# Performance work log

Hardware: AMD Instinct MI355X
Metric: run time of the kernel (lower is better)

The kernel has to match this reference:

```python
import jax, jax.numpy as jnp
import numpy as np

N = 100_000      # nodes
E = 1_600_000    # directed edges (before self-loops)
F_IN = 256       # input node features
H = 128          # hidden_dim
HEADS = 2
C_HEAD = H // HEADS  # 64, GATConv out_channels per head
G = 128          # graphs in batch
NCLS = 10
NEG_SLOPE = 0.2  # PyG GATConv default


def setup_inputs() -> dict:
    key = jax.random.key(0)
    ks = jax.random.split(key, 20)
    p = lambda k, shape: (jax.random.normal(k, shape, jnp.float32) * 0.05)
    x = jax.random.normal(ks[0], (N, F_IN), jnp.float32)
    edge_index = jax.random.randint(ks[1], (2, E), 0, N, dtype=jnp.int64)
    batch = jnp.sort(jax.random.randint(ks[2], (N,), 0, G, dtype=jnp.int64))
    return dict(
        x=x, edge_index=edge_index, batch=batch,
        pre_w=p(ks[3], (F_IN, H)), pre_b=p(ks[4], (H,)),
        w1=p(ks[5], (H, H)), asrc1=p(ks[6], (HEADS, C_HEAD)), adst1=p(ks[7], (HEADS, C_HEAD)), b1=p(ks[8], (H,)),
        w2=p(ks[9], (H, H)), asrc2=p(ks[10], (HEADS, C_HEAD)), adst2=p(ks[11], (HEADS, C_HEAD)), b2=p(ks[12], (H,)),
        post_w1=p(ks[13], (H, H)), post_b1=p(ks[14], (H,)),
        post_w2=p(ks[15], (H, NCLS)), post_b2=p(ks[16], (NCLS,)),
    )


def _gat_conv(h_in, w, a_src, a_dst, b, src, dst):
    # h: [N, heads, c]
    h = (h_in @ w).reshape(N, HEADS, C_HEAD)
    alpha_src = jnp.sum(h * a_src, axis=-1)  # [N, heads]
    alpha_dst = jnp.sum(h * a_dst, axis=-1)  # [N, heads]
    e = jax.nn.leaky_relu(alpha_src[src] + alpha_dst[dst], NEG_SLOPE)  # [E+N, heads]
    # numerically stable softmax over incoming edges of each destination node
    m = jax.ops.segment_max(e, dst, num_segments=N)
    ex = jnp.exp(e - m[dst])
    denom = jax.ops.segment_sum(ex, dst, num_segments=N)
    alpha = ex / denom[dst]                                           # [E+N, heads]
    out = jax.ops.segment_sum(h[src] * alpha[:, :, None], dst, num_segments=N)
    return out.reshape(N, H) + b  # concat heads + bias


def reference(x, edge_index, batch, pre_w, pre_b,
              w1, asrc1, adst1, b1, w2, asrc2, adst2, b2,
              post_w1, post_b1, post_w2, post_b2):
    # PyG GATConv default add_self_loops=True
    loop = jnp.arange(N, dtype=edge_index.dtype)
    src = jnp.concatenate([edge_index[0], loop])
    dst = jnp.concatenate([edge_index[1], loop])

    h = jax.nn.relu(x @ pre_w + pre_b)
    reprs = jax.ops.segment_sum(h, batch, num_segments=G)
    h = jax.nn.relu(_gat_conv(h, w1, asrc1, adst1, b1, src, dst))
    reprs = reprs + jax.ops.segment_sum(h, batch, num_segments=G)
    h = jax.nn.relu(_gat_conv(h, w2, asrc2, adst2, b2, src, dst))
    reprs = reprs + jax.ops.segment_sum(h, batch, num_segments=G)
    z = jax.nn.relu(reprs @ post_w1 + post_b1) @ post_w2 + post_b2
    return jax.nn.log_softmax(z, axis=-1)
```

## Files before the change

### kernel.cpp

```cpp
#include <hip/hip_runtime.h>
#include <hip/hip_bf16.h>
#include <math.h>

#define NNODES 100000
#define NEDGES 1600000
#define FIN 256
#define HDIM 128
#define NGRAPH 128
#define NCLS 10
#define NEG 0.2f

#define NBUCK 98
#define EPB 4096
#define EBLK ((NEDGES + EPB - 1) / EPB)

typedef short bf8 __attribute__((ext_vector_type(8)));
typedef float f4 __attribute__((ext_vector_type(4)));

__device__ __forceinline__ float lrelu(float x) { return x > 0.f ? x : NEG * x; }

__device__ __forceinline__ unsigned short f2bf(float f) {
  union { float f; unsigned int u; } v; v.f = f;
  unsigned int r = v.u + 0x7fffu + ((v.u >> 16) & 1u);
  return (unsigned short)(r >> 16);
}
__device__ __forceinline__ float bf_lo(unsigned int p) {
  union { unsigned int u; float f; } v; v.u = p << 16; return v.f;
}
__device__ __forceinline__ float bf_hi(unsigned int p) {
  union { unsigned int u; float f; } v; v.u = p & 0xffff0000u; return v.f;
}

__global__ __launch_bounds__(256) void convert_transpose(const float* __restrict__ w,
                                                         unsigned short* __restrict__ wt,
                                                         int K) {
  int i = blockIdx.x * 256 + threadIdx.x;
  if (i >= K * 128) return;
  int k = i >> 7, n = i & 127;
  wt[n * K + k] = f2bf(w[(size_t)k * 128 + n]);
}

__global__ __launch_bounds__(256) void gemm_mfma(const float* __restrict__ A,
                                                 const unsigned short* __restrict__ Bt,
                                                 const float* __restrict__ bias,
                                                 float* __restrict__ C,
                                                 unsigned int* __restrict__ Cp,
                                                 const float* __restrict__ a_src,
                                                 const float* __restrict__ a_dst,
                                                 float* __restrict__ o_as,
                                                 float* __restrict__ o_ad,
                                                 int M, int K, int dorelu) {
  __shared__ bf8 As[512];
  __shared__ bf8 Bs[512];
  int tid = threadIdx.x;
  int wv = tid >> 6, lane = tid & 63;
  int quad = lane >> 4, m16 = lane & 15;
  int row0 = blockIdx.x * 128;

  f4 acc[2][8];
#pragma unroll
  for (int a = 0; a < 2; ++a)
#pragma unroll
    for (int b = 0; b < 8; ++b) acc[a][b] = (f4){0.f, 0.f, 0.f, 0.f};

  for (int kb = 0; kb < K; kb += 32) {
    __syncthreads();
#pragma unroll
    for (int bb = 0; bb < 2; ++bb) {
      int b = tid + bb * 256;
      int l = b & 63, mt = b >> 6;
      int row = row0 + mt * 16 + (l & 15);
      if (row > M - 1) row = M - 1;
      const float* src = &A[(size_t)row * K + kb + (l >> 4) * 8];
      float4 x0 = *reinterpret_cast<const float4*>(src);
      float4 x1 = *reinterpret_cast<const float4*>(src + 4);
      bf8 v;
      v[0] = (short)f2bf(x0.x); v[1] = (short)f2bf(x0.y);
      v[2] = (short)f2bf(x0.z); v[3] = (short)f2bf(x0.w);
      v[4] = (short)f2bf(x1.x); v[5] = (short)f2bf(x1.y);
      v[6] = (short)f2bf(x1.z); v[7] = (short)f2bf(x1.w);
      As[b] = v;
    }
#pragma unroll
    for (int bb = 0; bb < 2; ++bb) {
      int b = tid + bb * 256;
      int l = b & 63, tn = b >> 6;
      int n = tn * 16 + (l & 15);
      Bs[b] = *reinterpret_cast<const bf8*>(&Bt[(size_t)n * K + kb + (l >> 4) * 8]);
    }
    __syncthreads();
    bf8 af0 = As[(wv * 2 + 0) * 64 + lane];
    bf8 af1 = As[(wv * 2 + 1) * 64 + lane];
#pragma unroll
    for (int tn = 0; tn < 8; ++tn) {
      bf8 bfm = Bs[tn * 64 + lane];
      acc[0][tn] = __builtin_amdgcn_mfma_f32_16x16x32_bf16(af0, bfm, acc[0][tn], 0, 0, 0);
      acc[1][tn] = __builtin_amdgcn_mfma_f32_16x16x32_bf16(af1, bfm, acc[1][tn], 0, 0, 0);
    }
  }

  if (Cp) {
    if (a_src) {
      float aS[8], aD[8];
#pragma unroll
      for (int tn = 0; tn < 4; ++tn) {
        aS[tn]     = a_src[tn * 16 + m16];
        aS[tn + 4] = a_src[64 + tn * 16 + m16];
        aD[tn]     = a_dst[tn * 16 + m16];
        aD[tn + 4] = a_dst[64 + tn * 16 + m16];
      }
#pragma unroll
      for (int mt = 0; mt < 2; ++mt)
#pragma unroll
        for (int r = 0; r < 4; ++r) {
          int row = row0 + wv * 32 + mt * 16 + quad * 4 + r;
          float ps0 = 0.f, ps1 = 0.f, pd0 = 0.f, pd1 = 0.f;
#pragma unroll
          for (int tn = 0; tn < 4; ++tn) {
            float v0 = acc[mt][tn][r], v1 = acc[mt][tn + 4][r];
            ps0 = fmaf(v0, aS[tn], ps0);
            ps1 = fmaf(v1, aS[tn + 4], ps1);
            pd0 = fmaf(v0, aD[tn], pd0);
            pd1 = fmaf(v1, aD[tn + 4], pd1);
          }
#pragma unroll
          for (int o = 8; o; o >>= 1) {
            ps0 += __shfl_xor(ps0, o); ps1 += __shfl_xor(ps1, o);
            pd0 += __shfl_xor(pd0, o); pd1 += __shfl_xor(pd1, o);
          }
          if (m16 == 0 && row < M) {
            o_as[2 * row] = ps0; o_as[2 * row + 1] = ps1;
            o_ad[2 * row] = pd0; o_ad[2 * row + 1] = pd1;
          }
        }
    }
#pragma unroll
    for (int mt = 0; mt < 2; ++mt)
#pragma unroll
      for (int tn = 0; tn < 4; ++tn)
#pragma unroll
        for (int r = 0; r < 4; ++r) {
          int row = row0 + wv * 32 + mt * 16 + quad * 4 + r;
          if (row < M) {
            unsigned int p = (unsigned int)f2bf(acc[mt][tn][r]) |
                             ((unsigned int)f2bf(acc[mt][tn + 4][r]) << 16);
            Cp[(size_t)row * 64 + tn * 16 + m16] = p;
          }
        }
  } else {
#pragma unroll
    for (int mt = 0; mt < 2; ++mt)
#pragma unroll
      for (int tn = 0; tn < 8; ++tn) {
        float bv = bias ? bias[tn * 16 + m16] : 0.f;
#pragma unroll
        for (int r = 0; r < 4; ++r) {
          int row = row0 + wv * 32 + mt * 16 + quad * 4 + r;
          if (row < M) {
            float v = acc[mt][tn][r] + bv;
            if (dorelu) v = fmaxf(v, 0.f);
            C[(size_t)row * 128 + tn * 16 + m16] = v;
          }
        }
      }
  }
}

__global__ void find_starts(const int* __restrict__ batch, int* __restrict__ gstart) {
  int g = threadIdx.x;
  if (g > NGRAPH) return;
  if (g == NGRAPH) { gstart[g] = NNODES; return; }
  int lo = 0, hi = NNODES;
  while (lo < hi) { int mid = (lo + hi) >> 1; if (batch[mid] < g) lo = mid + 1; else hi = mid; }
  gstart[g] = lo;
}

__global__ __launch_bounds__(256) void bin_count(const int* __restrict__ edst,
                                                 int* __restrict__ blockHist) {
  __shared__ int hist[NBUCK];
  int t = threadIdx.x, blk = blockIdx.x;
  if (t < NBUCK) hist[t] = 0;
  __syncthreads();
  int e0 = blk * EPB;
#pragma unroll
  for (int it = 0; it < EPB / 256; ++it) {
    int e = e0 + it * 256 + t;
    if (e < NEDGES) atomicAdd(&hist[((unsigned)edst[e]) >> 10], 1);
  }
  __syncthreads();
  if (t < NBUCK) blockHist[blk * NBUCK + t] = hist[t];
}

__global__ __launch_bounds__(512) void colscan(const int* __restrict__ blockHist,
                                               int* __restrict__ blockBaseCol,
                                               int* __restrict__ bucket_total) {
  __shared__ int s[512];
  int b = blockIdx.x, t = threadIdx.x;
  int v = (t < EBLK) ? blockHist[t * NBUCK + b] : 0;
  s[t] = v;
  __syncthreads();
  for (int off = 1; off < 512; off <<= 1) {
    int u = (t >= off) ? s[t - off] : 0;
    __syncthreads();
    s[t] += u;
    __syncthreads();
  }
  if (t < EBLK) blockBaseCol[b * EBLK + t] = s[t] - v;
  if (t == 511) bucket_total[b] = s[511];
}

__global__ __launch_bounds__(128) void bscan(const int* __restrict__ bucket_total,
                                             int* __restrict__ bucket_ptr) {
  __shared__ int s[128];
  int t = threadIdx.x;
  int v = (t < NBUCK) ? bucket_total[t] : 0;
  s[t] = v;
  __syncthreads();
  for (int off = 1; off < 128; off <<= 1) {
    int u = (t >= off) ? s[t - off] : 0;
    __syncthreads();
    s[t] += u;
    __syncthreads();
  }
  if (t < NBUCK) bucket_ptr[t] = s[t] - v;
  if (t == 127) bucket_ptr[NBUCK] = s[127];
}

__global__ __launch_bounds__(512) void bin_place(const int* __restrict__ esrc,
                                                 const int* __restrict__ edst,
                                                 const int* __restrict__ blockBaseCol,
                                                 const int* __restrict__ bucket_ptr,
                                                 uint2* __restrict__ stagingG) {
  __shared__ int hist[NBUCK + 1], lbase[NBUCK + 1], lcur[NBUCK + 1], cbase[NBUCK];
  __shared__ int tmp[128];
  __shared__ uint2 st[EPB];
  int t = threadIdx.x, blk = blockIdx.x;
  if (t < NBUCK + 1) hist[t] = 0;
  __syncthreads();
  int e0 = blk * EPB;
#pragma unroll
  for (int it = 0; it < EPB / 512; ++it) {
    int e = e0 + it * 512 + t;
    int b = NBUCK;
    if (e < NEDGES) b = ((unsigned)edst[e]) >> 10;
    atomicAdd(&hist[b], 1);
  }
  __syncthreads();
  if (t < 128) tmp[t] = (t < NBUCK + 1) ? hist[t] : 0;
  __syncthreads();
  for (int off = 1; off < 128; off <<= 1) {
    int u = 0;
    if (t < 128 && t >= off) u = tmp[t - off];
    __syncthreads();
    if (t < 128) tmp[t] += u;
    __syncthreads();
  }
  if (t < NBUCK + 1) { int ex = tmp[t] - hist[t]; lbase[t] = ex; lcur[t] = ex; }
  if (t < NBUCK) cbase[t] = bucket_ptr[t] + blockBaseCol[t * EBLK + blk];
  __syncthreads();
#pragma unroll
  for (int it = 0; it < EPB / 512; ++it) {
    int e = e0 + it * 512 + t;
    unsigned s = 0, d = 0xFFFFFFFFu;
    if (e < NEDGES) { s = (unsigned)esrc[e]; d = (unsigned)edst[e]; }
    int b = (d == 0xFFFFFFFFu) ? NBUCK : (int)(d >> 10);
    int slot = atomicAdd(&lcur[b], 1);
    st[slot] = make_uint2(s, d);
  }
  __syncthreads();
  for (int i = t; i < EPB; i += 512) {
    uint2 ed = st[i];
    if (ed.y == 0xFFFFFFFFu) continue;
    int b = (int)(ed.y >> 10);
    stagingG[cbase[b] + (i - lbase[b])] = ed;
  }
}

__global__ __launch_bounds__(1024) void bucket_deg_scan(const uint2* __restrict__ stagingG,
                                                        const int* __restrict__ bucket_ptr,
                                                        int* __restrict__ row_ptr) {
  __shared__ int dl[1024];
  int b = blockIdx.x, t = threadIdx.x;
  dl[t] = 0;
  __syncthreads();
  int s0 = bucket_ptr[b], s1 = bucket_ptr[b + 1];
  for (int j = s0 + t; j < s1; j += 1024)
    atomicAdd(&dl[stagingG[j].y & 1023], 1);
  __syncthreads();
  int myDeg = dl[t];
  for (int off = 1; off < 1024; off <<= 1) {
    int u = (t >= off) ? dl[t - off] : 0;
    __syncthreads();
    dl[t] += u;
    __syncthreads();
  }
  int excl = dl[t] - myDeg;
  int n = (b << 10) + t;
  if (n < NNODES) row_ptr[n] = s0 + excl;
  if (n == NNODES - 1) row_ptr[NNODES] = s0 + excl + myDeg;
}

__global__ __launch_bounds__(1024) void bucket_csr(const uint2* __restrict__ stagingG,
                                                   const int* __restrict__ bucket_ptr,
                                                   const int* __restrict__ row_ptr,
                                                   int* __restrict__ colv) {
  __shared__ int cur[1024];
  int b = blockIdx.x, t = threadIdx.x;
  int n = (b << 10) + t;
  cur[t] = (n < NNODES) ? row_ptr[n] : 0;
  __syncthreads();
  int s0 = bucket_ptr[b], s1 = bucket_ptr[b + 1];
  for (int j = s0 + t; j < s1; j += 1024) {
    uint2 e = stagingG[j];
    int pos = atomicAdd(&cur[e.y & 1023], 1);
    colv[pos] = (int)e.x;
  }
}

template<int T>
__device__ __forceinline__ void gather_T(const unsigned int* __restrict__ hwb,
                                         int lane, int sl, float w0l, float w1l,
                                         float& acc0, float& acc1) {
#pragma unroll
  for (int t = 0; t < T; ++t) {
    int s = __builtin_amdgcn_readlane(sl, t);
    float w0 = __uint_as_float(__builtin_amdgcn_readlane(__float_as_uint(w0l), t));
    float w1 = __uint_as_float(__builtin_amdgcn_readlane(__float_as_uint(w1l), t));
    unsigned q = hwb[(size_t)s * 64 + lane];
    acc0 = fmaf(w0, bf_lo(q), acc0);
    acc1 = fmaf(w1, bf_hi(q), acc1);
  }
}

__global__ __launch_bounds__(256) void aggregate(const unsigned int* __restrict__ hwb,
                                                 const float* __restrict__ a_s,
                                                 const float* __restrict__ a_d,
                                                 const int* __restrict__ row_ptr,
                                                 const int* __restrict__ colv,
                                                 const float* __restrict__ bias,
                                                 float* __restrict__ out) {
  int i = (blockIdx.x * 256 + threadIdx.x) >> 6;
  int lane = threadIdx.x & 63;
  if (i >= NNODES) return;
  float ad0 = a_d[2 * i], ad1 = a_d[2 * i + 1];
  float es0 = lrelu(a_s[2 * i] + ad0), es1 = lrelu(a_s[2 * i + 1] + ad1);
  int start = row_ptr[i], end = row_ptr[i + 1];
  int deg = end - start;

  int sl = 0; float e0l = -1e30f, e1l = -1e30f;
  if (lane < deg) {
    sl = colv[start + lane];
    float2 av = *reinterpret_cast<const float2*>(&a_s[2 * sl]);
    e0l = lrelu(av.x + ad0); e1l = lrelu(av.y + ad1);
  }
  float m0 = fmaxf(es0, e0l), m1 = fmaxf(es1, e1l);
  for (int j = start + 64 + lane; j < end; j += 64) {
    int s = colv[j];
    float2 av = *reinterpret_cast<const float2*>(&a_s[2 * s]);
    m0 = fmaxf(m0, lrelu(av.x + ad0));
    m1 = fmaxf(m1, lrelu(av.y + ad1));
  }
  for (int o = 32; o; o >>= 1) {
    m0 = fmaxf(m0, __shfl_xor(m0, o));
    m1 = fmaxf(m1, __shfl_xor(m1, o));
  }
  float w0l = lane < deg ? __expf(e0l - m0) : 0.f;
  float w1l = lane < deg ? __expf(e1l - m1) : 0.f;
  float d0 = w0l, d1 = w1l;
  for (int o = 32; o; o >>= 1) { d0 += __shfl_xor(d0, o); d1 += __shfl_xor(d1, o); }
  float ws0 = __expf(es0 - m0), ws1 = __expf(es1 - m1);
  float den0 = d0 + ws0, den1 = d1 + ws1;

  unsigned int ps = hwb[(size_t)i * 64 + lane];
  float acc0 = ws0 * bf_lo(ps), acc1 = ws1 * bf_hi(ps);
  int dmin = deg < 64 ? deg : 64;
  switch ((dmin + 7) >> 3) {
    case 1: gather_T<8 >(hwb, lane, sl, w0l, w1l, acc0, acc1); break;
    case 2: gather_T<16>(hwb, lane, sl, w0l, w1l, acc0, acc1); break;
    case 3: gather_T<24>(hwb, lane, sl, w0l, w1l, acc0, acc1); break;
    case 4: gather_T<32>(hwb, lane, sl, w0l, w1l, acc0, acc1); break;
    case 5: gather_T<40>(hwb, lane, sl, w0l, w1l, acc0, acc1); break;
    case 6: gather_T<48>(hwb, lane, sl, w0l, w1l, acc0, acc1); break;
    case 7: gather_T<56>(hwb, lane, sl, w0l, w1l, acc0, acc1); break;
    case 8: gather_T<64>(hwb, lane, sl, w0l, w1l, acc0, acc1); break;
    default: break;
  }
  for (int j = start + 64; j < end; ++j) {
    int s = colv[j];
    float2 av = *reinterpret_cast<const float2*>(&a_s[2 * s]);
    float w0 = __expf(lrelu(av.x + ad0) - m0);
    float w1 = __expf(lrelu(av.y + ad1) - m1);
    den0 += w0; den1 += w1;
    unsigned int q = hwb[(size_t)s * 64 + lane];
    acc0 = fmaf(w0, bf_lo(q), acc0);
    acc1 = fmaf(w1, bf_hi(q), acc1);
  }
  out[(size_t)i * 128 + lane]      = fmaxf(acc0 / den0 + bias[lane], 0.f);
  out[(size_t)i * 128 + 64 + lane] = fmaxf(acc1 / den1 + bias[64 + lane], 0.f);
}

#define SEG_CHUNK 128
__global__ __launch_bounds__(128) void seg_sum_fast(const float* __restrict__ h,
                                                    const int* __restrict__ batch,
                                                    const int* __restrict__ gstart,
                                                    float* __restrict__ reprs) {
  int n0 = blockIdx.x * SEG_CHUNK;
  if (n0 >= NNODES) return;
  int nend = n0 + SEG_CHUNK; if (nend > NNODES) nend = NNODES;
  int tid = threadIdx.x;
  int r = n0;
  while (r < nend) {
    int g = batch[r];
    int segend = gstart[g + 1]; if (segend > nend) segend = nend;
    float a0 = 0.f, a1 = 0.f, a2 = 0.f, a3 = 0.f;
    for (; r + 3 < segend; r += 4) {
      a0 += h[(size_t)r * 128 + tid];
      a1 += h[(size_t)(r + 1) * 128 + tid];
      a2 += h[(size_t)(r + 2) * 128 + tid];
      a3 += h[(size_t)(r + 3) * 128 + tid];
    }
    for (; r < segend; ++r) a0 += h[(size_t)r * 128 + tid];
    atomicAdd(&reprs[g * 128 + tid], (a0 + a1) + (a2 + a3));
  }
}

__global__ __launch_bounds__(128) void head_kernel(const float* __restrict__ reprs,
                                                   const float* __restrict__ pw1,
                                                   const float* __restrict__ pb1,
                                                   const float* __restrict__ pw2,
                                                   const float* __restrict__ pb2,
                                                   float* __restrict__ out) {
  __shared__ float r[128], t1[128], z[NCLS];
  int g = blockIdx.x, tid = threadIdx.x;
  r[tid] = reprs[g * 128 + tid];
  __syncthreads();
  float acc = pb1[tid];
  for (int k = 0; k < 128; ++k) acc = fmaf(r[k], pw1[k * 128 + tid], acc);
  t1[tid] = fmaxf(acc, 0.f);
  __syncthreads();
  if (tid < NCLS) {
    float zz = pb2[tid];
    for (int k = 0; k < 128; ++k) zz = fmaf(t1[k], pw2[k * NCLS + tid], zz);
    z[tid] = zz;
  }
  __syncthreads();
  if (tid == 0) {
    float mx = -1e30f;
    for (int c = 0; c < NCLS; ++c) mx = fmaxf(mx, z[c]);
    float s = 0.f;
    for (int c = 0; c < NCLS; ++c) s += expf(z[c] - mx);
    float ls = logf(s) + mx;
    for (int c = 0; c < NCLS; ++c) out[g * NCLS + c] = z[c] - ls;
  }
}

extern "C" void kernel_launch(void* const* d_in, const int* in_sizes, int n_in,
                              void* d_out, int out_size, void* d_ws, size_t ws_size,
                              hipStream_t stream) {
  const float* x     = (const float*)d_in[0];
  const int*   eidx  = (const int*)d_in[1];
  const int*   batch = (const int*)d_in[2];
  const float* pre_w = (const float*)d_in[3];
  const float* pre_b = (const float*)d_in[4];
  const float* w1    = (const float*)d_in[5];
  const float* asrc1 = (const float*)d_in[6];
  const float* adst1 = (const float*)d_in[7];
  const float* b1    = (const float*)d_in[8];
  const float* w2    = (const float*)d_in[9];
  const float* asrc2 = (const float*)d_in[10];
  const float* adst2 = (const float*)d_in[11];
  const float* b2    = (const float*)d_in[12];
  const float* pw1   = (const float*)d_in[13];
  const float* pb1   = (const float*)d_in[14];
  const float* pw2   = (const float*)d_in[15];
  const float* pb2   = (const float*)d_in[16];
  float* out = (float*)d_out;

  const int* esrc = eidx;
  const int* edst = eidx + NEDGES;

  char* wsp = (char*)d_ws;
  size_t off = 0;
  auto alloc = [&](size_t bytes) -> void* {
    void* p = wsp + off;
    off += (bytes + 255) & ~(size_t)255;
    return p;
  };
  float* h          = (float*)alloc((size_t)NNODES * 128 * 4);
  unsigned int* hwb = (unsigned int*)alloc((size_t)NNODES * 64 * 4);
  float* a_s        = (float*)alloc((size_t)NNODES * 2 * 4);
  float* a_d        = (float*)alloc((size_t)NNODES * 2 * 4);
  float* reprs      = (float*)alloc((size_t)NGRAPH * 128 * 4);
  int* gstart       = (int*)alloc((NGRAPH + 1) * 4);
  int* row_ptr      = (int*)alloc(((size_t)NNODES + 1) * 4);
  int* colv         = (int*)alloc((size_t)NEDGES * 4);
  unsigned short* wt_pre = (unsigned short*)alloc((size_t)128 * FIN * 2);
  unsigned short* wt1    = (unsigned short*)alloc((size_t)128 * HDIM * 2);
  unsigned short* wt2    = (unsigned short*)alloc((size_t)128 * HDIM * 2);
  int* blockHist    = (int*)alloc((size_t)EBLK * NBUCK * 4);
  int* blockBaseCol = (int*)alloc((size_t)NBUCK * EBLK * 4);
  int* bucket_total = (int*)alloc(NBUCK * 4);
  int* bucket_ptr   = (int*)alloc((NBUCK + 1) * 4);
  uint2* stagingG   = (uint2*)alloc((size_t)NEDGES * 8);

  int wb = NNODES / 4;
  int sb = (NNODES + SEG_CHUNK - 1) / SEG_CHUNK;
  int gb = (NNODES + 127) / 128;

  convert_transpose<<<(FIN * 128 + 255) / 256, 256, 0, stream>>>(pre_w, wt_pre, FIN);
  convert_transpose<<<(HDIM * 128 + 255) / 256, 256, 0, stream>>>(w1, wt1, HDIM);
  convert_transpose<<<(HDIM * 128 + 255) / 256, 256, 0, stream>>>(w2, wt2, HDIM);

  hipMemsetAsync(reprs, 0, (size_t)NGRAPH * 128 * 4, stream);
  find_starts<<<1, 256, 0, stream>>>(batch, gstart);

  bin_count<<<EBLK, 256, 0, stream>>>(edst, blockHist);
  colscan<<<NBUCK, 512, 0, stream>>>(blockHist, blockBaseCol, bucket_total);
  bscan<<<1, 128, 0, stream>>>(bucket_total, bucket_ptr);
  bin_place<<<EBLK, 512, 0, stream>>>(esrc, edst, blockBaseCol, bucket_ptr, stagingG);
  bucket_deg_scan<<<NBUCK, 1024, 0, stream>>>(stagingG, bucket_ptr, row_ptr);
  bucket_csr<<<NBUCK, 1024, 0, stream>>>(stagingG, bucket_ptr, row_ptr, colv);

  gemm_mfma<<<gb, 256, 0, stream>>>(x, wt_pre, pre_b, h, nullptr,
                                    nullptr, nullptr, nullptr, nullptr, NNODES, FIN, 1);
  seg_sum_fast<<<sb, 128, 0, stream>>>(h, batch, gstart, reprs);

  gemm_mfma<<<gb, 256, 0, stream>>>(h, wt1, nullptr, nullptr, hwb,
                                    asrc1, adst1, a_s, a_d, NNODES, HDIM, 0);
  aggregate<<<wb, 256, 0, stream>>>(hwb, a_s, a_d, row_ptr, colv, b1, h);
  seg_sum_fast<<<sb, 128, 0, stream>>>(h, batch, gstart, reprs);

  gemm_mfma<<<gb, 256, 0, stream>>>(h, wt2, nullptr, nullptr, hwb,
                                    asrc2, adst2, a_s, a_d, NNODES, HDIM, 0);
  aggregate<<<wb, 256, 0, stream>>>(hwb, a_s, a_d, row_ptr, colv, b2, h);
  seg_sum_fast<<<sb, 128, 0, stream>>>(h, batch, gstart, reprs);

  head_kernel<<<NGRAPH, 128, 0, stream>>>(reprs, pw1, pb1, pw2, pb2, out);
}
```

Baseline: 528.2 us.

## Store hidden activations in bf16, pack staging edges, fuse CSR build kernels

```diff
diff --git a/kernel.cpp b/kernel.cpp
--- a/kernel.cpp
+++ b/kernel.cpp
@@ -24,6 +24,9 @@
   unsigned int r = v.u + 0x7fffu + ((v.u >> 16) & 1u);
   return (unsigned short)(r >> 16);
 }
+__device__ __forceinline__ float bf2f(unsigned short u) {
+  union { unsigned int u; float f; } v; v.u = ((unsigned int)u) << 16; return v.f;
+}
 __device__ __forceinline__ float bf_lo(unsigned int p) {
   union { unsigned int u; float f; } v; v.u = p << 16; return v.f;
 }
@@ -40,10 +43,11 @@
   wt[n * K + k] = f2bf(w[(size_t)k * 128 + n]);
 }
 
-__global__ __launch_bounds__(256) void gemm_mfma(const float* __restrict__ A,
+__global__ __launch_bounds__(256) void gemm_mfma(const void* __restrict__ Av,
+                                                 int a_bf16,
                                                  const unsigned short* __restrict__ Bt,
                                                  const float* __restrict__ bias,
-                                                 float* __restrict__ C,
+                                                 unsigned short* __restrict__ Cb,
                                                  unsigned int* __restrict__ Cp,
                                                  const float* __restrict__ a_src,
                                                  const float* __restrict__ a_dst,
@@ -71,15 +75,21 @@
       int l = b & 63, mt = b >> 6;
       int row = row0 + mt * 16 + (l & 15);
       if (row > M - 1) row = M - 1;
-      const float* src = &A[(size_t)row * K + kb + (l >> 4) * 8];
-      float4 x0 = *reinterpret_cast<const float4*>(src);
-      float4 x1 = *reinterpret_cast<const float4*>(src + 4);
-      bf8 v;
-      v[0] = (short)f2bf(x0.x); v[1] = (short)f2bf(x0.y);
-      v[2] = (short)f2bf(x0.z); v[3] = (short)f2bf(x0.w);
-      v[4] = (short)f2bf(x1.x); v[5] = (short)f2bf(x1.y);
-      v[6] = (short)f2bf(x1.z); v[7] = (short)f2bf(x1.w);
-      As[b] = v;
+      if (a_bf16) {
+        const unsigned short* src =
+            (const unsigned short*)Av + (size_t)row * K + kb + (l >> 4) * 8;
+        As[b] = *reinterpret_cast<const bf8*>(src);
+      } else {
+        const float* src = (const float*)Av + (size_t)row * K + kb + (l >> 4) * 8;
+        float4 x0 = *reinterpret_cast<const float4*>(src);
+        float4 x1 = *reinterpret_cast<const float4*>(src + 4);
+        bf8 v;
+        v[0] = (short)f2bf(x0.x); v[1] = (short)f2bf(x0.y);
+        v[2] = (short)f2bf(x0.z); v[3] = (short)f2bf(x0.w);
+        v[4] = (short)f2bf(x1.x); v[5] = (short)f2bf(x1.y);
+        v[6] = (short)f2bf(x1.z); v[7] = (short)f2bf(x1.w);
+        As[b] = v;
+      }
     }
 #pragma unroll
     for (int bb = 0; bb < 2; ++bb) {
@@ -159,7 +169,7 @@
           if (row < M) {
             float v = acc[mt][tn][r] + bv;
             if (dorelu) v = fmaxf(v, 0.f);
-            C[(size_t)row * 128 + tn * 16 + m16] = v;
+            Cb[(size_t)row * 128 + tn * 16 + m16] = f2bf(v);
           }
         }
       }
@@ -230,7 +240,7 @@
                                                  const int* __restrict__ edst,
                                                  const int* __restrict__ blockBaseCol,
                                                  const int* __restrict__ bucket_ptr,
-                                                 uint2* __restrict__ stagingG) {
+                                                 unsigned* __restrict__ stagingG) {
   __shared__ int hist[NBUCK + 1], lbase[NBUCK + 1], lcur[NBUCK + 1], cbase[NBUCK];
   __shared__ int tmp[128];
   __shared__ uint2 st[EPB];
@@ -272,20 +282,22 @@
     uint2 ed = st[i];
     if (ed.y == 0xFFFFFFFFu) continue;
     int b = (int)(ed.y >> 10);
-    stagingG[cbase[b] + (i - lbase[b])] = ed;
-  }
-}
-
-__global__ __launch_bounds__(1024) void bucket_deg_scan(const uint2* __restrict__ stagingG,
-                                                        const int* __restrict__ bucket_ptr,
-                                                        int* __restrict__ row_ptr) {
+    stagingG[cbase[b] + (i - lbase[b])] = ((ed.y & 1023u) << 17) | ed.x;
+  }
+}
+
+__global__ __launch_bounds__(1024) void bucket_csr_fused(const unsigned* __restrict__ stagingG,
+                                                         const int* __restrict__ bucket_ptr,
+                                                         int* __restrict__ row_ptr,
+                                                         int* __restrict__ colv) {
   __shared__ int dl[1024];
+  __shared__ int cur[1024];
   int b = blockIdx.x, t = threadIdx.x;
   dl[t] = 0;
   __syncthreads();
   int s0 = bucket_ptr[b], s1 = bucket_ptr[b + 1];
   for (int j = s0 + t; j < s1; j += 1024)
-    atomicAdd(&dl[stagingG[j].y & 1023], 1);
+    atomicAdd(&dl[stagingG[j] >> 17], 1);
   __syncthreads();
   int myDeg = dl[t];
   for (int off = 1; off < 1024; off <<= 1) {
@@ -294,26 +306,16 @@
     dl[t] += u;
     __syncthreads();
   }
-  int excl = dl[t] - myDeg;
+  int rp = s0 + dl[t] - myDeg;
+  cur[t] = rp;
   int n = (b << 10) + t;
-  if (n < NNODES) row_ptr[n] = s0 + excl;
-  if (n == NNODES - 1) row_ptr[NNODES] = s0 + excl + myDeg;
-}
-
-__global__ __launch_bounds__(1024) void bucket_csr(const uint2* __restrict__ stagingG,
-                                                   const int* __restrict__ bucket_ptr,
-                                                   const int* __restrict__ row_ptr,
-                                                   int* __restrict__ colv) {
-  __shared__ int cur[1024];
-  int b = blockIdx.x, t = threadIdx.x;
-  int n = (b << 10) + t;
-  cur[t] = (n < NNODES) ? row_ptr[n] : 0;
-  __syncthreads();
-  int s0 = bucket_ptr[b], s1 = bucket_ptr[b + 1];
+  if (n < NNODES) row_ptr[n] = rp;
+  if (n == NNODES - 1) row_ptr[NNODES] = rp + myDeg;
+  __syncthreads();
   for (int j = s0 + t; j < s1; j += 1024) {
-    uint2 e = stagingG[j];
-    int pos = atomicAdd(&cur[e.y & 1023], 1);
-    colv[pos] = (int)e.x;
+    unsigned v = stagingG[j];
+    int pos = atomicAdd(&cur[v >> 17], 1);
+    colv[pos] = (int)(v & 0x1FFFFu);
   }
 }
 
@@ -338,7 +340,7 @@
                                                  const int* __restrict__ row_ptr,
                                                  const int* __restrict__ colv,
                                                  const float* __restrict__ bias,
-                                                 float* __restrict__ out) {
+                                                 unsigned short* __restrict__ out) {
   int i = (blockIdx.x * 256 + threadIdx.x) >> 6;
   int lane = threadIdx.x & 63;
   if (i >= NNODES) return;
@@ -395,12 +397,12 @@
     acc0 = fmaf(w0, bf_lo(q), acc0);
     acc1 = fmaf(w1, bf_hi(q), acc1);
   }
-  out[(size_t)i * 128 + lane]      = fmaxf(acc0 / den0 + bias[lane], 0.f);
-  out[(size_t)i * 128 + 64 + lane] = fmaxf(acc1 / den1 + bias[64 + lane], 0.f);
+  out[(size_t)i * 128 + lane]      = f2bf(fmaxf(acc0 / den0 + bias[lane], 0.f));
+  out[(size_t)i * 128 + 64 + lane] = f2bf(fmaxf(acc1 / den1 + bias[64 + lane], 0.f));
 }
 
 #define SEG_CHUNK 128
-__global__ __launch_bounds__(128) void seg_sum_fast(const float* __restrict__ h,
+__global__ __launch_bounds__(128) void seg_sum_fast(const unsigned short* __restrict__ h,
                                                     const int* __restrict__ batch,
                                                     const int* __restrict__ gstart,
                                                     float* __restrict__ reprs) {
@@ -414,12 +416,12 @@
     int segend = gstart[g + 1]; if (segend > nend) segend = nend;
     float a0 = 0.f, a1 = 0.f, a2 = 0.f, a3 = 0.f;
     for (; r + 3 < segend; r += 4) {
-      a0 += h[(size_t)r * 128 + tid];
-      a1 += h[(size_t)(r + 1) * 128 + tid];
-      a2 += h[(size_t)(r + 2) * 128 + tid];
-      a3 += h[(size_t)(r + 3) * 128 + tid];
+      a0 += bf2f(h[(size_t)r * 128 + tid]);
+      a1 += bf2f(h[(size_t)(r + 1) * 128 + tid]);
+      a2 += bf2f(h[(size_t)(r + 2) * 128 + tid]);
+      a3 += bf2f(h[(size_t)(r + 3) * 128 + tid]);
     }
-    for (; r < segend; ++r) a0 += h[(size_t)r * 128 + tid];
+    for (; r < segend; ++r) a0 += bf2f(h[(size_t)r * 128 + tid]);
     atomicAdd(&reprs[g * 128 + tid], (a0 + a1) + (a2 + a3));
   }
 }
@@ -486,22 +488,22 @@
     off += (bytes + 255) & ~(size_t)255;
     return p;
   };
-  float* h          = (float*)alloc((size_t)NNODES * 128 * 4);
-  unsigned int* hwb = (unsigned int*)alloc((size_t)NNODES * 64 * 4);
-  float* a_s        = (float*)alloc((size_t)NNODES * 2 * 4);
-  float* a_d        = (float*)alloc((size_t)NNODES * 2 * 4);
-  float* reprs      = (float*)alloc((size_t)NGRAPH * 128 * 4);
-  int* gstart       = (int*)alloc((NGRAPH + 1) * 4);
-  int* row_ptr      = (int*)alloc(((size_t)NNODES + 1) * 4);
-  int* colv         = (int*)alloc((size_t)NEDGES * 4);
+  unsigned short* hb = (unsigned short*)alloc((size_t)NNODES * 128 * 2);
+  unsigned int* hwb  = (unsigned int*)alloc((size_t)NNODES * 64 * 4);
+  float* a_s         = (float*)alloc((size_t)NNODES * 2 * 4);
+  float* a_d         = (float*)alloc((size_t)NNODES * 2 * 4);
+  float* reprs       = (float*)alloc((size_t)NGRAPH * 128 * 4);
+  int* gstart        = (int*)alloc((NGRAPH + 1) * 4);
+  int* row_ptr       = (int*)alloc(((size_t)NNODES + 1) * 4);
+  int* colv          = (int*)alloc((size_t)NEDGES * 4);
   unsigned short* wt_pre = (unsigned short*)alloc((size_t)128 * FIN * 2);
   unsigned short* wt1    = (unsigned short*)alloc((size_t)128 * HDIM * 2);
   unsigned short* wt2    = (unsigned short*)alloc((size_t)128 * HDIM * 2);
-  int* blockHist    = (int*)alloc((size_t)EBLK * NBUCK * 4);
-  int* blockBaseCol = (int*)alloc((size_t)NBUCK * EBLK * 4);
-  int* bucket_total = (int*)alloc(NBUCK * 4);
-  int* bucket_ptr   = (int*)alloc((NBUCK + 1) * 4);
-  uint2* stagingG   = (uint2*)alloc((size_t)NEDGES * 8);
+  int* blockHist     = (int*)alloc((size_t)EBLK * NBUCK * 4);
+  int* blockBaseCol  = (int*)alloc((size_t)NBUCK * EBLK * 4);
+  int* bucket_total  = (int*)alloc(NBUCK * 4);
+  int* bucket_ptr    = (int*)alloc((NBUCK + 1) * 4);
+  unsigned* stagingG = (unsigned*)alloc((size_t)NEDGES * 4);
 
   int wb = NNODES / 4;
   int sb = (NNODES + SEG_CHUNK - 1) / SEG_CHUNK;
@@ -518,22 +520,21 @@
   colscan<<<NBUCK, 512, 0, stream>>>(blockHist, blockBaseCol, bucket_total);
   bscan<<<1, 128, 0, stream>>>(bucket_total, bucket_ptr);
   bin_place<<<EBLK, 512, 0, stream>>>(esrc, edst, blockBaseCol, bucket_ptr, stagingG);
-  bucket_deg_scan<<<NBUCK, 1024, 0, stream>>>(stagingG, bucket_ptr, row_ptr);
-  bucket_csr<<<NBUCK, 1024, 0, stream>>>(stagingG, bucket_ptr, row_ptr, colv);
-
-  gemm_mfma<<<gb, 256, 0, stream>>>(x, wt_pre, pre_b, h, nullptr,
+  bucket_csr_fused<<<NBUCK, 1024, 0, stream>>>(stagingG, bucket_ptr, row_ptr, colv);
+
+  gemm_mfma<<<gb, 256, 0, stream>>>(x, 0, wt_pre, pre_b, hb, nullptr,
                                     nullptr, nullptr, nullptr, nullptr, NNODES, FIN, 1);
-  seg_sum_fast<<<sb, 128, 0, stream>>>(h, batch, gstart, reprs);
-
-  gemm_mfma<<<gb, 256, 0, stream>>>(h, wt1, nullptr, nullptr, hwb,
+  seg_sum_fast<<<sb, 128, 0, stream>>>(hb, batch, gstart, reprs);
+
+  gemm_mfma<<<gb, 256, 0, stream>>>(hb, 1, wt1, nullptr, nullptr, hwb,
                                     asrc1, adst1, a_s, a_d, NNODES, HDIM, 0);
-  aggregate<<<wb, 256, 0, stream>>>(hwb, a_s, a_d, row_ptr, colv, b1, h);
-  seg_sum_fast<<<sb, 128, 0, stream>>>(h, batch, gstart, reprs);
-
-  gemm_mfma<<<gb, 256, 0, stream>>>(h, wt2, nullptr, nullptr, hwb,
+  aggregate<<<wb, 256, 0, stream>>>(hwb, a_s, a_d, row_ptr, colv, b1, hb);
+  seg_sum_fast<<<sb, 128, 0, stream>>>(hb, batch, gstart, reprs);
+
+  gemm_mfma<<<gb, 256, 0, stream>>>(hb, 1, wt2, nullptr, nullptr, hwb,
                                     asrc2, adst2, a_s, a_d, NNODES, HDIM, 0);
-  aggregate<<<wb, 256, 0, stream>>>(hwb, a_s, a_d, row_ptr, colv, b2, h);
-  seg_sum_fast<<<sb, 128, 0, stream>>>(h, batch, gstart, reprs);
+  aggregate<<<wb, 256, 0, stream>>>(hwb, a_s, a_d, row_ptr, colv, b2, hb);
+  seg_sum_fast<<<sb, 128, 0, stream>>>(hb, batch, gstart, reprs);
 
   head_kernel<<<NGRAPH, 128, 0, stream>>>(reprs, pw1, pb1, pw2, pb2, out);
 }
```

Result: faster. 513.2 us (-2.9%).
